# Kernel tuning notes

Hardware: AMD Instinct MI355X
Metric: run time of the kernel (lower is better)

## Reference

```python
import jax
import jax.numpy as jnp
import numpy as np
from jax import lax

# Grid / problem dimensions (match init_kwargs / input_specs)
B = 1          # batch_size
D, H, W = 16, 128, 128   # full-resolution voxel grid (z, y, x)
N = 120000     # number of occupied voxels
CIN = 16       # num_input_features
EPS = 1e-5     # MinkowskiBatchNorm eps (eval mode, running stats)


def setup_inputs() -> dict:
    key = jax.random.key(0)
    ks = jax.random.split(key, 24)

    # Unique voxel coordinates (ME.SparseTensor coordinates are unique after quantization)
    perm = jax.random.permutation(ks[0], D * H * W)[:N]
    z = (perm // (H * W)).astype(jnp.int32)
    y = ((perm // W) % H).astype(jnp.int32)
    x = (perm % W).astype(jnp.int32)
    coors = jnp.stack([jnp.zeros(N, jnp.int32), z, y, x], axis=1)  # (batch, z, y, x)

    voxel_features = jax.random.normal(ks[1], (N, CIN), jnp.float32)

    def w(k, shape, fan_in):
        return jax.random.normal(k, shape, jnp.float32) * (1.0 / np.sqrt(fan_in))

    w0 = w(ks[2], (32, 16, 3, 3, 3), 16 * 27)
    w1 = w(ks[3], (32, 32, 3, 3, 3), 32 * 27)
    w2 = w(ks[4], (64, 32, 3, 3, 3), 32 * 27)
    w64 = w(ks[5], (7, 64, 64, 3, 3, 3), 64 * 27)   # the seven 64->64 k=3^3 convs
    w10 = w(ks[6], (64, 64, 3, 1, 1), 64 * 3)        # final k=(3,1,1) conv

    bn32_gamma = 1.0 + 0.1 * jax.random.normal(ks[7], (2, 32), jnp.float32)
    bn32_beta = 0.1 * jax.random.normal(ks[8], (2, 32), jnp.float32)
    bn32_mean = 0.1 * jax.random.normal(ks[9], (2, 32), jnp.float32)
    bn32_var = 0.5 + jax.random.uniform(ks[10], (2, 32), jnp.float32)
    bn64_gamma = 1.0 + 0.1 * jax.random.normal(ks[11], (9, 64), jnp.float32)
    bn64_beta = 0.1 * jax.random.normal(ks[12], (9, 64), jnp.float32)
    bn64_mean = 0.1 * jax.random.normal(ks[13], (9, 64), jnp.float32)
    bn64_var = 0.5 + jax.random.uniform(ks[14], (9, 64), jnp.float32)

    return {
        "voxel_features": voxel_features, "coors": coors,
        "w0": w0, "w1": w1, "w2": w2, "w64": w64, "w10": w10,
        "bn32_gamma": bn32_gamma, "bn32_beta": bn32_beta,
        "bn32_mean": bn32_mean, "bn32_var": bn32_var,
        "bn64_gamma": bn64_gamma, "bn64_beta": bn64_beta,
        "bn64_mean": bn64_mean, "bn64_var": bn64_var,
        "batch_size": B,
    }


def _conv(x, w, stride_z):
    # Minkowski conv with odd kernel is a centered conv; in the z-downsampled
    # dense grid, kernel offsets scaled by tensor stride reduce to ordinary
    # dense conv with 'half' padding per axis and stride on z.
    pads = [(w.shape[2] // 2,) * 2, (w.shape[3] // 2,) * 2, (w.shape[4] // 2,) * 2]
    return lax.conv_general_dilated(
        x, w, (stride_z, 1, 1), pads,
        dimension_numbers=("NCDHW", "OIDHW", "NCDHW"))


def _bn_relu(x, g, b, m, v):
    inv = g / jnp.sqrt(v + EPS)                    # [C]
    sh = (1, -1, 1, 1, 1)
    return jax.nn.relu(x * inv.reshape(sh) + (b - m * inv).reshape(sh))


def _pool_z(occ):
    # strided Minkowski conv output coords = unique(floor(c/2)) of input coords
    return jnp.maximum(occ[:, :, 0::2], occ[:, :, 1::2])


def reference(voxel_features, coors, w0, w1, w2, w64, w10,
              bn32_gamma, bn32_beta, bn32_mean, bn32_var,
              bn64_gamma, bn64_beta, bn64_mean, bn64_var, batch_size):
    b, z, y, x = coors[:, 0], coors[:, 1], coors[:, 2], coors[:, 3]
    # Densify sparse tensor (unoccupied voxels are exact zeros, as in ME)
    h = jnp.zeros((batch_size, D, H, W, CIN), voxel_features.dtype)
    h = h.at[b, z, y, x].set(voxel_features)
    h = jnp.moveaxis(h, -1, 1)                                   # [B,C,D,H,W]
    occ = jnp.zeros((batch_size, 1, D, H, W), voxel_features.dtype)
    occ = occ.at[b, 0, z, y, x].set(1.0)

    # Two 32-channel stride-1 convs: output coords == input coords -> mask with occ
    h = _bn_relu(_conv(h, w0, 1), bn32_gamma[0], bn32_beta[0], bn32_mean[0], bn32_var[0]) * occ
    h = _bn_relu(_conv(h, w1, 1), bn32_gamma[1], bn32_beta[1], bn32_mean[1], bn32_var[1]) * occ

    # 32->64, stride (2,1,1)
    occ = _pool_z(occ)
    h = _bn_relu(_conv(h, w2, 2), bn64_gamma[0], bn64_beta[0], bn64_mean[0], bn64_var[0]) * occ
    # three 64->64 stride-1 convs
    for i in range(3):
        h = _bn_relu(_conv(h, w64[i], 1), bn64_gamma[1 + i], bn64_beta[1 + i], bn64_mean[1 + i], bn64_var[1 + i]) * occ
    # 64->64 stride (2,1,1)
    occ = _pool_z(occ)
    h = _bn_relu(_conv(h, w64[3], 2), bn64_gamma[4], bn64_beta[4], bn64_mean[4], bn64_var[4]) * occ
    # three 64->64 stride-1 convs
    for i in range(3):
        h = _bn_relu(_conv(h, w64[4 + i], 1), bn64_gamma[5 + i], bn64_beta[5 + i], bn64_mean[5 + i], bn64_var[5 + i]) * occ
    # final 64->64, kernel (3,1,1), stride (2,1,1)
    occ = _pool_z(occ)
    h = _bn_relu(_conv(h, w10, 2), bn64_gamma[8], bn64_beta[8], bn64_mean[8], bn64_var[8]) * occ

    # prune is a no-op (all coords in-range by construction); dense() -> [B,C,Dz,H,W]
    n, c, d, hh, ww = h.shape
    return h.reshape(n, c * d, hh, ww)
```

## Files before the change

kernel.cpp:

```cpp
#include <hip/hip_runtime.h>

#define HW 16384

typedef _Float16 half8  __attribute__((ext_vector_type(8)));
typedef _Float16 half4v __attribute__((ext_vector_type(4)));
typedef float    f32x4  __attribute__((ext_vector_type(4)));

typedef __attribute__((address_space(3))) unsigned int lds_u32;
typedef const __attribute__((address_space(1))) unsigned int glb_u32;

__device__ __forceinline__ void gl_lds16(const void* g, void* l) {
    __builtin_amdgcn_global_load_lds((glb_u32*)g, (lds_u32*)l, 16, 0, 0);
}

__global__ void zero4(float4* __restrict__ p, int n4) {
    int i = blockIdx.x * 256 + threadIdx.x;
    if (i < n4) p[i] = make_float4(0.f, 0.f, 0.f, 0.f);
}

__global__ void write_code_f32(float* out, float v) {
    if (threadIdx.x == 0 && blockIdx.x == 0) out[0] = v;
}

__global__ void border_zero(_Float16* __restrict__ base, int D, int CS) {
    int idx = blockIdx.x * 256 + threadIdx.x;
    int gpc = CS / 8;
    int total = D * 516 * gpc;
    if (idx >= total) return;
    int g = idx % gpc;
    int c = (idx / gpc) % 516;
    int d = idx / (gpc * 516);
    int y, x;
    if (c < 130)      { y = 0;           x = c; }
    else if (c < 260) { y = 129;         x = c - 130; }
    else if (c < 388) { y = c - 260 + 1; x = 0; }
    else              { y = c - 388 + 1; x = 129; }
    *(float4*)(base + ((size_t)(d * 130 + y) * 130 + x) * CS + g * 8) =
        make_float4(0.f, 0.f, 0.f, 0.f);
}

struct PackDesc {
    const float* src[11];
    int dstoff[11];
    int cum[12];
    int cinr[11];
    int cinp[11];
    int cout[11];
    int khw[11];
};

__global__ void pack_all(PackDesc pd, _Float16* __restrict__ AP) {
    int u = blockIdx.x * 256 + threadIdx.x;
    if (u >= pd.cum[11]) return;
    int s = 0;
    while (u >= pd.cum[s + 1]) ++s;
    int idx = u - pd.cum[s];
    const int CINr = pd.cinr[s], CINp = pd.cinp[s], KHW = pd.khw[s];
    const int KD = 3;
    const int NSTEPS = KD * KHW * KHW * (CINp / 32);
    const float* W = pd.src[s];
    int lane = idx & 63;
    int st   = (idx >> 6) % NSTEPS;
    int grp  = idx / (NSTEPS * 64);
    int k0  = st * 32 + (lane >> 4) * 8;
    int t   = k0 / CINp;
    int ci0 = k0 % CINp;
    int co  = grp * 16 + (lane & 15);
    int khw2 = KHW * KHW;
    int dz = t / khw2, r = t % khw2, dy = r / KHW, dx = r % KHW;
    half8 hv;
    for (int j = 0; j < 8; ++j) {
        int ci = ci0 + j;
        float wv = (ci < CINr)
            ? W[(((size_t)co * CINr + ci) * KD + dz) * khw2 + dy * KHW + dx] : 0.0f;
        hv[j] = (_Float16)wv;
    }
    *(half8*)(AP + pd.dstoff[s] + ((size_t)(grp * NSTEPS + st) * 64 + lane) * 8) = hv;
}

__global__ void scatter_f16(const float* __restrict__ vf, const int* __restrict__ coors,
                            _Float16* __restrict__ act, unsigned char* __restrict__ occ, int n) {
    int i = blockIdx.x * 256 + threadIdx.x;
    if (i >= n) return;
    int z = coors[i * 4 + 1];
    int y = coors[i * 4 + 2];
    int x = coors[i * 4 + 3];
    size_t cell = ((size_t)(z * 130 + (y + 1)) * 130 + (x + 1)) * 40;
    for (int c = 0; c < 16; ++c) act[cell + c] = (_Float16)vf[i * 16 + c];
    occ[z * HW + y * 128 + x] = 1;
}

__global__ void pool_occ(const unsigned char* __restrict__ o0, unsigned char* __restrict__ o1,
                         unsigned char* __restrict__ o2, unsigned char* __restrict__ o3) {
    int p = blockIdx.x * 256 + threadIdx.x;
    if (p >= HW) return;
    unsigned char a[16];
    for (int z = 0; z < 16; ++z) a[z] = o0[z * HW + p];
    for (int z = 0; z < 8; ++z) { a[z] = a[2 * z] | a[2 * z + 1]; o1[z * HW + p] = a[z]; }
    for (int z = 0; z < 4; ++z) { a[z] = a[2 * z] | a[2 * z + 1]; o2[z * HW + p] = a[z]; }
    for (int z = 0; z < 2; ++z) { a[z] = a[2 * z] | a[2 * z + 1]; o3[z * HW + p] = a[z]; }
}

template <int CINp, int COUT, int KD, int KHW, int SZ, int DIN, int DOUT, bool FINAL>
__global__ __launch_bounds__(256, 2)
void conv_mfma(const _Float16* __restrict__ act, const _Float16* __restrict__ apack,
               const float* __restrict__ gm, const float* __restrict__ bt,
               const float* __restrict__ mn, const float* __restrict__ vr,
               const unsigned char* __restrict__ occ, void* __restrict__ outv) {
    constexpr int PADXY  = KHW / 2;
    constexpr int CB     = CINp / 32;
    constexpr int MG     = COUT / 16;
    constexpr int NSTEPS = KD * KHW * KHW * CB;
    constexpr int CS     = CINp + 8;
    constexpr int OCS    = COUT + 8;
    constexpr int NGRAN  = 4 * 130 * CS / 8;
    constexpr int NIT    = (NGRAN + 255) / 256;
    constexpr int OFS    = 1 - PADXY;
    constexpr int NWG    = DOUT * 64;

    __shared__ _Float16 smem[4 * 130 * CS];

    const int bid0 = blockIdx.x;
    const int bid = (bid0 & 7) * (NWG / 8) + (bid0 >> 3);
    const int yp = bid & 63;
    const int z0 = bid >> 6;
    const int y0 = yp * 2;
    const int tid  = threadIdx.x;
    const int w    = tid >> 6;
    const int lane = tid & 63;
    const int ylocal = w >> 1;
    const int x0w    = (w & 1) * 64;
    const int n  = lane & 15;
    const int kg = lane >> 4;

    f32x4 acc[MG][4];
    #pragma unroll
    for (int m = 0; m < MG; ++m)
        #pragma unroll
        for (int t = 0; t < 4; ++t) { acc[m][t][0] = 0.f; acc[m][t][1] = 0.f; acc[m][t][2] = 0.f; acc[m][t][3] = 0.f; }

    const int zb = z0 * SZ;
    const int dzlo = (zb == 0) ? 1 : 0;
    const int dzhi = (zb + KD - 1 > DIN) ? (KD - 1) : KD;

    for (int dz = dzlo; dz < dzhi; ++dz) {
        const int zi = zb + dz - 1;
        __syncthreads();
        const _Float16* src = act + (size_t)(zi * 130 + y0) * (130 * CS);
        #pragma unroll
        for (int it = 0; it < NIT; ++it) {
            int g = it * 256 + tid;
            if (g < NGRAN) gl_lds16(src + (size_t)g * 8, smem + (size_t)g * 8);
        }
        asm volatile("s_waitcnt vmcnt(0)" ::: "memory");
        __syncthreads();
        #pragma unroll
        for (int dy = 0; dy < KHW; ++dy) {
            #pragma unroll
            for (int dx = 0; dx < KHW; ++dx) {
                #pragma unroll
                for (int cb = 0; cb < CB; ++cb) {
                    const int sabs = dz * (KHW * KHW * CB) + (dy * KHW + dx) * CB + cb;
                    half8 a[MG];
                    #pragma unroll
                    for (int mg = 0; mg < MG; ++mg)
                        a[mg] = *(const half8*)(apack + ((size_t)(mg * NSTEPS + sabs) * 64 + lane) * 8);
                    const _Float16* bp = smem
                        + ((ylocal + dy + OFS) * 130 + x0w + n + dx + OFS) * CS + cb * 32 + kg * 8;
                    #pragma unroll
                    for (int nt = 0; nt < 4; ++nt) {
                        half8 b = *(const half8*)(bp + nt * 16 * CS);
                        #pragma unroll
                        for (int mg = 0; mg < MG; ++mg)
                            acc[mg][nt] = __builtin_amdgcn_mfma_f32_16x16x32_f16(a[mg], b, acc[mg][nt], 0, 0, 0);
                    }
                }
            }
        }
    }

    const int yo = y0 + ylocal;
    #pragma unroll
    for (int mg = 0; mg < MG; ++mg) {
        const int co0 = mg * 16 + kg * 4;
        const f32x4 gv = *(const f32x4*)(gm + co0);
        const f32x4 bv = *(const f32x4*)(bt + co0);
        const f32x4 mv = *(const f32x4*)(mn + co0);
        const f32x4 vv = *(const f32x4*)(vr + co0);
        float sc[4], sh[4];
        #pragma unroll
        for (int r = 0; r < 4; ++r) {
            sc[r] = gv[r] * __frsqrt_rn(vv[r] + 1e-5f);
            sh[r] = bv[r] - mv[r] * sc[r];
        }
        #pragma unroll
        for (int nt = 0; nt < 4; ++nt) {
            const int x = x0w + nt * 16 + n;
            const float occv = (float)occ[z0 * HW + yo * 128 + x];
            float v0 = fmaxf(fmaf(acc[mg][nt][0], sc[0], sh[0]), 0.f) * occv;
            float v1 = fmaxf(fmaf(acc[mg][nt][1], sc[1], sh[1]), 0.f) * occv;
            float v2 = fmaxf(fmaf(acc[mg][nt][2], sc[2], sh[2]), 0.f) * occv;
            float v3 = fmaxf(fmaf(acc[mg][nt][3], sc[3], sh[3]), 0.f) * occv;
            if constexpr (FINAL) {
                float* o = (float*)outv;
                const int sp = yo * 128 + x;
                o[((size_t)(co0 + 0) * 2 + z0) * HW + sp] = v0;
                o[((size_t)(co0 + 1) * 2 + z0) * HW + sp] = v1;
                o[((size_t)(co0 + 2) * 2 + z0) * HW + sp] = v2;
                o[((size_t)(co0 + 3) * 2 + z0) * HW + sp] = v3;
            } else {
                _Float16* o = (_Float16*)outv;
                half4v hv;
                hv[0] = (_Float16)v0; hv[1] = (_Float16)v1;
                hv[2] = (_Float16)v2; hv[3] = (_Float16)v3;
                *(half4v*)(o + ((size_t)(z0 * 130 + (yo + 1)) * 130 + (x + 1)) * OCS + co0) = hv;
            }
        }
    }
}

extern "C" void kernel_launch(void* const* d_in, const int* in_sizes, int n_in,
                              void* d_out, int out_size, void* d_ws, size_t ws_size,
                              hipStream_t stream) {
    const float* vf    = (const float*)d_in[0];
    const int*   coors = (const int*)d_in[1];
    const float* w0    = (const float*)d_in[2];
    const float* w1    = (const float*)d_in[3];
    const float* w2    = (const float*)d_in[4];
    const float* w64   = (const float*)d_in[5];
    const float* w10   = (const float*)d_in[6];
    const float* g32   = (const float*)d_in[7];
    const float* b32   = (const float*)d_in[8];
    const float* m32   = (const float*)d_in[9];
    const float* v32   = (const float*)d_in[10];
    const float* g64   = (const float*)d_in[11];
    const float* b64   = (const float*)d_in[12];
    const float* m64   = (const float*)d_in[13];
    const float* v64   = (const float*)d_in[14];
    const int N = in_sizes[0] / 16;

    float* out_f = (float*)d_out;

    const size_t R0 = 0;
    const size_t R1 = 21632000;
    const size_t R3 = 43264000;
    const size_t OFF_OCC0 = 62732800;
    const size_t OFF_OCC1 = 62994944;
    const size_t OFF_OCC2 = 63126016;
    const size_t OFF_OCC3 = 63191552;
    const size_t OFF_AP   = 63224320;
    const size_t TOTAL_BYTES = 65018368;

    if (ws_size < TOTAL_BYTES) {
        write_code_f32<<<dim3(1), dim3(64), 0, stream>>>(out_f, 1.0e8f);
        return;
    }

    char* wsb = (char*)d_ws;
    _Float16* A0p = (_Float16*)(wsb + R0);
    _Float16* A1p = (_Float16*)(wsb + R1);
    _Float16* A3p = (_Float16*)(wsb + R3);
    _Float16* A2p = A1p;
    unsigned char* occ0 = (unsigned char*)(wsb + OFF_OCC0);
    unsigned char* occ1 = (unsigned char*)(wsb + OFF_OCC1);
    unsigned char* occ2 = (unsigned char*)(wsb + OFF_OCC2);
    unsigned char* occ3 = (unsigned char*)(wsb + OFF_OCC3);
    _Float16* AP = (_Float16*)(wsb + OFF_AP);

    const size_t W_A0 = 0, W_A1 = 27648, W_A2 = 55296, W_A3 = 110592, W_A10 = 884736;

    zero4<<<dim3((21632000 / 16 + 255) / 256), dim3(256), 0, stream>>>((float4*)(wsb + R0), 21632000 / 16);
    zero4<<<dim3((262144 / 16 + 255) / 256), dim3(256), 0, stream>>>((float4*)occ0, 262144 / 16);
    {
        int t1 = 16 * 516 * (40 / 8);
        border_zero<<<dim3((t1 + 255) / 256), dim3(256), 0, stream>>>(A1p, 16, 40);
        int t3 = 8 * 516 * (72 / 8);
        border_zero<<<dim3((t3 + 255) / 256), dim3(256), 0, stream>>>(A3p, 8, 72);
    }

    {
        PackDesc pd;
        int units[11] = {3456, 3456, 6912, 13824, 13824, 13824, 13824, 13824, 13824, 13824, 1536};
        const float* srcs[11] = {w0, w1, w2,
                                 w64 + 0 * 110592, w64 + 1 * 110592, w64 + 2 * 110592,
                                 w64 + 3 * 110592, w64 + 4 * 110592, w64 + 5 * 110592,
                                 w64 + 6 * 110592, w10};
        int offs[11] = {(int)W_A0, (int)W_A1, (int)W_A2,
                        (int)(W_A3 + 0 * 110592), (int)(W_A3 + 1 * 110592), (int)(W_A3 + 2 * 110592),
                        (int)(W_A3 + 3 * 110592), (int)(W_A3 + 4 * 110592), (int)(W_A3 + 5 * 110592),
                        (int)(W_A3 + 6 * 110592), (int)W_A10};
        int cinr[11] = {16, 32, 32, 64, 64, 64, 64, 64, 64, 64, 64};
        int cinp[11] = {32, 32, 32, 64, 64, 64, 64, 64, 64, 64, 64};
        int cout[11] = {32, 32, 64, 64, 64, 64, 64, 64, 64, 64, 64};
        int khw[11]  = {3, 3, 3, 3, 3, 3, 3, 3, 3, 3, 1};
        int c = 0;
        for (int i = 0; i < 11; ++i) {
            pd.src[i] = srcs[i]; pd.dstoff[i] = offs[i]; pd.cum[i] = c; c += units[i];
            pd.cinr[i] = cinr[i]; pd.cinp[i] = cinp[i]; pd.cout[i] = cout[i]; pd.khw[i] = khw[i];
        }
        pd.cum[11] = c;
        pack_all<<<dim3((c + 255) / 256), dim3(256), 0, stream>>>(pd, AP);
    }

    scatter_f16<<<dim3((N + 255) / 256), dim3(256), 0, stream>>>(vf, coors, A0p, occ0, N);
    pool_occ<<<dim3(HW / 256), dim3(256), 0, stream>>>(occ0, occ1, occ2, occ3);

    conv_mfma<32, 32, 3, 3, 1, 16, 16, false><<<dim3(16 * 64), dim3(256), 0, stream>>>(
        A0p, AP + W_A0, g32, b32, m32, v32, occ0, A1p);
    conv_mfma<32, 32, 3, 3, 1, 16, 16, false><<<dim3(16 * 64), dim3(256), 0, stream>>>(
        A1p, AP + W_A1, g32 + 32, b32 + 32, m32 + 32, v32 + 32, occ0, A0p);
    {
        int t = 8 * 516 * (72 / 8);
        border_zero<<<dim3((t + 255) / 256), dim3(256), 0, stream>>>(A2p, 8, 72);
    }
    conv_mfma<32, 64, 3, 3, 2, 16, 8, false><<<dim3(8 * 64), dim3(256), 0, stream>>>(
        A0p, AP + W_A2, g64, b64, m64, v64, occ1, A2p);
    {
        int t = 4 * 516 * (72 / 8);
        border_zero<<<dim3((t + 255) / 256), dim3(256), 0, stream>>>(A0p, 4, 72);
    }
    conv_mfma<64, 64, 3, 3, 1, 8, 8, false><<<dim3(8 * 64), dim3(256), 0, stream>>>(
        A2p, AP + W_A3 + 0 * 110592, g64 + 64, b64 + 64, m64 + 64, v64 + 64, occ1, A3p);
    conv_mfma<64, 64, 3, 3, 1, 8, 8, false><<<dim3(8 * 64), dim3(256), 0, stream>>>(
        A3p, AP + W_A3 + 1 * 110592, g64 + 128, b64 + 128, m64 + 128, v64 + 128, occ1, A2p);
    conv_mfma<64, 64, 3, 3, 1, 8, 8, false><<<dim3(8 * 64), dim3(256), 0, stream>>>(
        A2p, AP + W_A3 + 2 * 110592, g64 + 192, b64 + 192, m64 + 192, v64 + 192, occ1, A3p);
    conv_mfma<64, 64, 3, 3, 2, 8, 4, false><<<dim3(4 * 64), dim3(256), 0, stream>>>(
        A3p, AP + W_A3 + 3 * 110592, g64 + 256, b64 + 256, m64 + 256, v64 + 256, occ2, A0p);
    {
        int t = 4 * 516 * (72 / 8);
        border_zero<<<dim3((t + 255) / 256), dim3(256), 0, stream>>>(A1p, 4, 72);
    }
    conv_mfma<64, 64, 3, 3, 1, 4, 4, false><<<dim3(4 * 64), dim3(256), 0, stream>>>(
        A0p, AP + W_A3 + 4 * 110592, g64 + 320, b64 + 320, m64 + 320, v64 + 320, occ2, A1p);
    conv_mfma<64, 64, 3, 3, 1, 4, 4, false><<<dim3(4 * 64), dim3(256), 0, stream>>>(
        A1p, AP + W_A3 + 5 * 110592, g64 + 384, b64 + 384, m64 + 384, v64 + 384, occ2, A0p);
    conv_mfma<64, 64, 3, 3, 1, 4, 4, false><<<dim3(4 * 64), dim3(256), 0, stream>>>(
        A0p, AP + W_A3 + 6 * 110592, g64 + 448, b64 + 448, m64 + 448, v64 + 448, occ2, A1p);
    conv_mfma<64, 64, 3, 1, 2, 4, 2, true><<<dim3(2 * 64), dim3(256), 0, stream>>>(
        A1p, AP + W_A10, g64 + 512, b64 + 512, m64 + 512, v64 + 512, occ3, out_f);
}
```

Before: 349.8 us.

## Double-buffer LDS activation slices across depth taps in conv kernel

Splits the LDS staging buffer into two halves so the next z-slice is prefetched with global_load_lds while MFMA work runs on the current slice. A partial vmcnt wait replaces the full drain before each compute phase. Launch bounds drop to one block per CU, since the doubled LDS footprint (close to the LDS limit for the 64-channel layers) rules out two resident blocks. The per-granule bounds guard is removed, so each stage over-reads up to a padded count past the slice, and occupancy-based latency hiding is traded for explicit overlap.

After: 442.4 us. 26.5% more time.

```diff
diff --git a/kernel.cpp b/kernel.cpp
--- a/kernel.cpp
+++ b/kernel.cpp
@@ -11,6 +11,13 @@
 
 __device__ __forceinline__ void gl_lds16(const void* g, void* l) {
     __builtin_amdgcn_global_load_lds((glb_u32*)g, (lds_u32*)l, 16, 0, 0);
+}
+
+template <int N> __device__ __forceinline__ void wait_vm() {
+    static_assert(N == 0 || N == 11 || N == 19, "unsupported vmcnt literal");
+    if constexpr (N == 0)  asm volatile("s_waitcnt vmcnt(0)" ::: "memory");
+    if constexpr (N == 11) asm volatile("s_waitcnt vmcnt(11)" ::: "memory");
+    if constexpr (N == 19) asm volatile("s_waitcnt vmcnt(19)" ::: "memory");
 }
 
 __global__ void zero4(float4* __restrict__ p, int n4) {
@@ -102,7 +109,7 @@
 }
 
 template <int CINp, int COUT, int KD, int KHW, int SZ, int DIN, int DOUT, bool FINAL>
-__global__ __launch_bounds__(256, 2)
+__global__ __launch_bounds__(256, 1)
 void conv_mfma(const _Float16* __restrict__ act, const _Float16* __restrict__ apack,
                const float* __restrict__ gm, const float* __restrict__ bt,
                const float* __restrict__ mn, const float* __restrict__ vr,
@@ -114,11 +121,12 @@
     constexpr int CS     = CINp + 8;
     constexpr int OCS    = COUT + 8;
     constexpr int NGRAN  = 4 * 130 * CS / 8;
-    constexpr int NIT    = (NGRAN + 255) / 256;
+    constexpr int G      = (NGRAN + 255) / 256;
+    constexpr int GP     = G * 256;
     constexpr int OFS    = 1 - PADXY;
     constexpr int NWG    = DOUT * 64;
 
-    __shared__ _Float16 smem[4 * 130 * CS];
+    __shared__ _Float16 smem[2][GP * 8];
 
     const int bid0 = blockIdx.x;
     const int bid = (bid0 & 7) * (NWG / 8) + (bid0 >> 3);
@@ -143,17 +151,26 @@
     const int dzlo = (zb == 0) ? 1 : 0;
     const int dzhi = (zb + KD - 1 > DIN) ? (KD - 1) : KD;
 
+    auto stage = [&](int bufi, int dz) {
+        const int zi = zb + dz - 1;
+        const _Float16* src = act + (size_t)(zi * 130 + y0) * (130 * CS);
+        _Float16* dst = &smem[bufi][0];
+        #pragma unroll
+        for (int it = 0; it < G; ++it) {
+            const size_t g = (size_t)it * 256 + tid;
+            gl_lds16(src + g * 8, dst + g * 8);
+        }
+    };
+
+    stage(0, dzlo);
+    int cur = 0;
     for (int dz = dzlo; dz < dzhi; ++dz) {
-        const int zi = zb + dz - 1;
+        const bool has_next = (dz + 1 < dzhi);
+        if (dz > dzlo) __syncthreads();
+        if (has_next) stage(cur ^ 1, dz + 1);
+        if (has_next) wait_vm<G>(); else wait_vm<0>();
         __syncthreads();
-        const _Float16* src = act + (size_t)(zi * 130 + y0) * (130 * CS);
-        #pragma unroll
-        for (int it = 0; it < NIT; ++it) {
-            int g = it * 256 + tid;
-            if (g < NGRAN) gl_lds16(src + (size_t)g * 8, smem + (size_t)g * 8);
-        }
-        asm volatile("s_waitcnt vmcnt(0)" ::: "memory");
-        __syncthreads();
+        const _Float16* sm = &smem[cur][0];
         #pragma unroll
         for (int dy = 0; dy < KHW; ++dy) {
             #pragma unroll
@@ -165,7 +182,7 @@
                     #pragma unroll
                     for (int mg = 0; mg < MG; ++mg)
                         a[mg] = *(const half8*)(apack + ((size_t)(mg * NSTEPS + sabs) * 64 + lane) * 8);
-                    const _Float16* bp = smem
+                    const _Float16* bp = sm
                         + ((ylocal + dy + OFS) * 130 + x0w + n + dx + OFS) * CS + cb * 32 + kg * 8;
                     #pragma unroll
                     for (int nt = 0; nt < 4; ++nt) {
@@ -177,6 +194,7 @@
                 }
             }
         }
+        cur ^= 1;
     }
 
     const int yo = y0 + ylocal;
```
